# Performance work log

Measured on AMD Instinct MI355X. Metric: run time of the kernel, lower is better.

The kernel has to match this reference:

```python
import jax, jax.numpy as jnp
import numpy as np

EPS = 1e-6

def l2norm(x):
    return x / jnp.maximum(jnp.linalg.norm(x, axis=-1, keepdims=True), 1e-12)

def setup_inputs() -> dict:
    key = jax.random.key(0)
    ks = jax.random.split(key, 16)
    B, V, L = 64, 197, 64
    Dv, Dt, E = 768, 768, 256
    s = (2.0 / E) ** 0.5  # kaiming fan_out scale
    inp = {
        'visual_cls': jax.random.normal(ks[0], (B, Dv), jnp.float32),
        'textual_cls': jax.random.normal(ks[1], (B, Dt), jnp.float32),
        'visual_tokens': jax.random.normal(ks[2], (B, V, Dv), jnp.float32),
        'textual_tokens': jax.random.normal(ks[3], (B, L, Dt), jnp.float32),
        'text_length': jnp.maximum(jax.random.randint(ks[4], (B,), 0, L, jnp.int32), 1),
        'Wv': jax.random.normal(ks[5], (Dv, E), jnp.float32) * s,
        'bv': jnp.zeros((E,), jnp.float32),
        'Wt': jax.random.normal(ks[6], (Dt, E), jnp.float32) * s,
        'bt': jnp.zeros((E,), jnp.float32),
        'Wvt': jax.random.normal(ks[7], (Dv, E), jnp.float32) * s,
        'bvt': jnp.zeros((E,), jnp.float32),
        'Wtt': jax.random.normal(ks[8], (Dt, E), jnp.float32) * s,
        'btt': jnp.zeros((E,), jnp.float32),
    }
    return inp

def reference(visual_cls, textual_cls, visual_tokens, textual_tokens, text_length,
              Wv, bv, Wt, bt, Wvt, bvt, Wtt, btt):
    # cls projections
    v_cls = visual_cls @ Wv + bv            # [B, E]
    t_cls = textual_cls @ Wt + bt           # [B, E]
    # token projections + l2 normalize
    v_tok = l2norm(visual_tokens @ Wvt + bvt)   # [B, V, E]
    t_tok = l2norm(textual_tokens @ Wtt + btt)  # [B, L, E]
    B, V, E = v_tok.shape
    L = t_tok.shape[1]
    # full cross-modal token similarity (this is the kernel target)
    sim = jnp.einsum('bvd,qtd->bqvt', v_tok, t_tok)  # [B, Q, V, T]
    # image->text: max over text tokens, plain mean over visual tokens
    image_to_text = jnp.max(sim, axis=-1)            # [B, Q, V]
    image_to_text_sim = jnp.sum(image_to_text, axis=-1) / V  # [B, Q]
    # text->image: max over visual tokens, masked mean over text tokens
    text_to_image = jnp.max(sim, axis=-2)            # [B, Q, T]
    # faithful to original: mask indexed by FIRST batch axis b
    mask = jnp.arange(L)[None, :] >= text_length[:, None]   # [B, T]
    mask3 = mask[:, None, :]                                 # [B, 1, T]
    numer = jnp.sum(jnp.where(mask3, 0.0, text_to_image), axis=-1)
    denom = jnp.maximum(jnp.sum(~mask3, axis=-1).astype(text_to_image.dtype), EPS)
    text_to_image_sim = numer / denom                # [B, Q]
    return (v_cls, t_cls, image_to_text_sim, text_to_image_sim)
```

## Files before the change

### kernel.cpp

```cpp
#include <hip/hip_runtime.h>
#include <hip/hip_bf16.h>

#define NB 64
#define NV 197
#define NL 64
#define ND 768
#define NE 256

typedef __attribute__((ext_vector_type(8))) short bh8;
typedef __attribute__((ext_vector_type(16))) float f32x16;

__device__ inline ushort f2bf(float x) {
  __hip_bfloat16 h = __float2bfloat16(x);
  return *reinterpret_cast<ushort*>(&h);
}

__device__ inline bh8 cvt8(float4 a, float4 b) {
  union { bh8 v; ushort u[8]; } r;
  r.u[0] = f2bf(a.x); r.u[1] = f2bf(a.y); r.u[2] = f2bf(a.z); r.u[3] = f2bf(a.w);
  r.u[4] = f2bf(b.x); r.u[5] = f2bf(b.y); r.u[6] = f2bf(b.z); r.u[7] = f2bf(b.w);
  return r.v;
}

__global__ __launch_bounds__(128, 2) void proj_kernel(
    const float* __restrict__ Xv, const float* __restrict__ Xt,
    const float* __restrict__ Xcv, const float* __restrict__ Xct,
    const float* __restrict__ Wvt, const float* __restrict__ Wtt,
    const float* __restrict__ Wv, const float* __restrict__ Wt,
    const float* __restrict__ bvt, const float* __restrict__ btt,
    const float* __restrict__ bv, const float* __restrict__ bt,
    ushort* __restrict__ v_tok, ushort* __restrict__ t_tok,
    float* __restrict__ v_cls, float* __restrict__ t_cls) {
  __shared__ float ssq_lds[2][32];

  const int blk = blockIdx.x;
  const float* X; const float* W; const float* bias;
  ushort* outb = nullptr; float* outf = nullptr;
  int row0; bool norm;
  if (blk < 394)      { X = Xv;  W = Wvt; bias = bvt; outb = v_tok; row0 = blk * 32;         norm = true; }
  else if (blk < 522) { X = Xt;  W = Wtt; bias = btt; outb = t_tok; row0 = (blk - 394) * 32; norm = true; }
  else if (blk < 524) { X = Xcv; W = Wv;  bias = bv;  outf = v_cls; row0 = (blk - 522) * 32; norm = false; }
  else                { X = Xct; W = Wt;  bias = bt;  outf = t_cls; row0 = (blk - 524) * 32; norm = false; }

  const int tid = threadIdx.x;
  const int l = tid & 63, w = tid >> 6;
  const int lr = l & 31, hi = l >> 5;

  const float* Arow = X + (size_t)(row0 + lr) * ND + hi * 8;
  const float* Wcol = W + w * 128 + lr;

  f32x16 acc0 = {0}, acc1 = {0}, acc2 = {0}, acc3 = {0};

#pragma unroll 2
  for (int ks = 0; ks < 48; ++ks) {
    const float* Ak = Arow + ks * 16;
    float4 a0 = *(const float4*)Ak;
    float4 a1 = *(const float4*)(Ak + 4);
    bh8 af = cvt8(a0, a1);

    const float* Bk = Wcol + (size_t)(ks * 16 + hi * 8) * NE;
    union { bh8 v; ushort u[8]; } b0, b1, b2, b3;
#pragma unroll
    for (int e = 0; e < 8; ++e) {
      const float* Be = Bk + (size_t)e * NE;
      b0.u[e] = f2bf(Be[0]);
      b1.u[e] = f2bf(Be[32]);
      b2.u[e] = f2bf(Be[64]);
      b3.u[e] = f2bf(Be[96]);
    }
    acc0 = __builtin_amdgcn_mfma_f32_32x32x16_bf16(af, b0.v, acc0, 0, 0, 0);
    acc1 = __builtin_amdgcn_mfma_f32_32x32x16_bf16(af, b1.v, acc1, 0, 0, 0);
    acc2 = __builtin_amdgcn_mfma_f32_32x32x16_bf16(af, b2.v, acc2, 0, 0, 0);
    acc3 = __builtin_amdgcn_mfma_f32_32x32x16_bf16(af, b3.v, acc3, 0, 0, 0);
  }

  const float bn0 = bias[w * 128 + lr];
  const float bn1 = bias[w * 128 + 32 + lr];
  const float bn2 = bias[w * 128 + 64 + lr];
  const float bn3 = bias[w * 128 + 96 + lr];
#pragma unroll
  for (int r = 0; r < 16; ++r) {
    acc0[r] += bn0; acc1[r] += bn1; acc2[r] += bn2; acc3[r] += bn3;
  }

  if (norm) {
    float p[16];
#pragma unroll
    for (int r = 0; r < 16; ++r)
      p[r] = acc0[r] * acc0[r] + acc1[r] * acc1[r] +
             acc2[r] * acc2[r] + acc3[r] * acc3[r];
#pragma unroll
    for (int off = 1; off < 32; off <<= 1) {
#pragma unroll
      for (int r = 0; r < 16; ++r) p[r] += __shfl_xor(p[r], off);
    }
    if (lr == 0) {
#pragma unroll
      for (int r = 0; r < 16; ++r)
        ssq_lds[w][(r & 3) + 8 * (r >> 2) + 4 * hi] = p[r];
    }
    __syncthreads();
#pragma unroll
    for (int r = 0; r < 16; ++r) {
      const int R = (r & 3) + 8 * (r >> 2) + 4 * hi;
      const float s = ssq_lds[0][R] + ssq_lds[1][R];
      const float scale = 1.0f / fmaxf(sqrtf(s), 1e-12f);
      ushort* orow = outb + (size_t)(row0 + R) * NE + w * 128 + lr;
      orow[0]  = f2bf(acc0[r] * scale);
      orow[32] = f2bf(acc1[r] * scale);
      orow[64] = f2bf(acc2[r] * scale);
      orow[96] = f2bf(acc3[r] * scale);
    }
  } else {
#pragma unroll
    for (int r = 0; r < 16; ++r) {
      const int R = (r & 3) + 8 * (r >> 2) + 4 * hi;
      float* orow = outf + (size_t)(row0 + R) * NE + w * 128 + lr;
      orow[0]  = acc0[r];
      orow[32] = acc1[r];
      orow[64] = acc2[r];
      orow[96] = acc3[r];
    }
  }
}

__global__ __launch_bounds__(256, 2) void sim_kernel(
    const __hip_bfloat16* __restrict__ vt,
    const __hip_bfloat16* __restrict__ tt,
    const int* __restrict__ tlen,
    float* __restrict__ out_i2t,
    float* __restrict__ out_t2i) {
  __shared__ float red[4 * 64];
  __shared__ float wsum[4];

  const int blk = blockIdx.x;
  const int q = blk & 63;
  const int bc = blk >> 6;
  const int tid = threadIdx.x;
  const int l = tid & 63;
  const int w = tid >> 6;
  const int lr = l & 31;
  const int hi = l >> 5;

  bh8 breg0[16], breg1[16];
  {
    const __hip_bfloat16* T0 = tt + ((size_t)(q * NL) + lr) * NE + hi * 8;
    const __hip_bfloat16* T1 = T0 + 32 * NE;
#pragma unroll
    for (int s = 0; s < 16; ++s) {
      breg0[s] = *(const bh8*)(T0 + s * 16);
      breg1[s] = *(const bh8*)(T1 + s * 16);
    }
  }

  const int r0 = 32 * w + lr;
  const int r1 = min(128 + 32 * w + lr, NV - 1);

  for (int ib = 0; ib < 8; ++ib) {
    const int b = bc * 8 + ib;
    const __hip_bfloat16* Vb = vt + (size_t)b * NV * NE + hi * 8;
    const __hip_bfloat16* A0 = Vb + (size_t)r0 * NE;
    const __hip_bfloat16* A1 = Vb + (size_t)r1 * NE;

    f32x16 acc00 = {0}, acc01 = {0}, acc10 = {0}, acc11 = {0};

    bh8 a0[4], a1[4];
#pragma unroll
    for (int s = 0; s < 4; ++s) {
      a0[s] = *(const bh8*)(A0 + s * 16);
      a1[s] = *(const bh8*)(A1 + s * 16);
    }
#pragma unroll
    for (int s = 0; s < 16; ++s) {
      bh8 va0 = a0[s & 3], va1 = a1[s & 3];
      if (s < 12) {
        a0[s & 3] = *(const bh8*)(A0 + (s + 4) * 16);
        a1[s & 3] = *(const bh8*)(A1 + (s + 4) * 16);
      }
      acc00 = __builtin_amdgcn_mfma_f32_32x32x16_bf16(va0, breg0[s], acc00, 0, 0, 0);
      acc01 = __builtin_amdgcn_mfma_f32_32x32x16_bf16(va0, breg1[s], acc01, 0, 0, 0);
      acc10 = __builtin_amdgcn_mfma_f32_32x32x16_bf16(va1, breg0[s], acc10, 0, 0, 0);
      acc11 = __builtin_amdgcn_mfma_f32_32x32x16_bf16(va1, breg1[s], acc11, 0, 0, 0);
    }

    float i2t_sum = 0.0f;
#pragma unroll
    for (int r = 0; r < 16; ++r) {
      {
        float m = fmaxf(acc00[r], acc01[r]);
        m = fmaxf(m, __shfl_xor(m, 1));
        m = fmaxf(m, __shfl_xor(m, 2));
        m = fmaxf(m, __shfl_xor(m, 4));
        m = fmaxf(m, __shfl_xor(m, 8));
        m = fmaxf(m, __shfl_xor(m, 16));
        i2t_sum += m;
      }
      {
        float m = fmaxf(acc10[r], acc11[r]);
        m = fmaxf(m, __shfl_xor(m, 1));
        m = fmaxf(m, __shfl_xor(m, 2));
        m = fmaxf(m, __shfl_xor(m, 4));
        m = fmaxf(m, __shfl_xor(m, 8));
        m = fmaxf(m, __shfl_xor(m, 16));
        const int row = 128 + 32 * w + (r & 3) + 8 * (r >> 2) + 4 * hi;
        if (row < NV) i2t_sum += m;
      }
    }
    i2t_sum += __shfl_xor(i2t_sum, 32);
    if (l == 0) wsum[w] = i2t_sum;

    float vm0 = -1e30f, vm1 = -1e30f;
#pragma unroll
    for (int r = 0; r < 16; ++r) {
      vm0 = fmaxf(vm0, fmaxf(acc00[r], acc10[r]));
      vm1 = fmaxf(vm1, fmaxf(acc01[r], acc11[r]));
    }
    vm0 = fmaxf(vm0, __shfl_xor(vm0, 32));
    vm1 = fmaxf(vm1, __shfl_xor(vm1, 32));
    if (hi == 0) red[w * 64 + lr] = vm0;
    else         red[w * 64 + 32 + lr] = vm1;

    __syncthreads();

    if (tid < 64) {
      const int len = tlen[b];
      float m = fmaxf(fmaxf(red[tid], red[64 + tid]),
                      fmaxf(red[128 + tid], red[192 + tid]));
      float v = (tid < len) ? m : 0.0f;
#pragma unroll
      for (int off = 1; off < 64; off <<= 1) v += __shfl_xor(v, off);
      if (tid == 0) {
        out_t2i[b * NB + q] = v / fmaxf((float)len, 1e-6f);
        out_i2t[b * NB + q] = (wsum[0] + wsum[1] + wsum[2] + wsum[3]) / (float)NV;
      }
    }
    __syncthreads();
  }
}

extern "C" void kernel_launch(void* const* d_in, const int* in_sizes, int n_in,
                              void* d_out, int out_size, void* d_ws, size_t ws_size,
                              hipStream_t stream) {
  (void)in_sizes; (void)n_in; (void)out_size; (void)ws_size;
  const float* visual_cls    = (const float*)d_in[0];
  const float* textual_cls   = (const float*)d_in[1];
  const float* visual_tokens = (const float*)d_in[2];
  const float* textual_tokens= (const float*)d_in[3];
  const int*   text_length   = (const int*)d_in[4];
  const float* Wv  = (const float*)d_in[5];
  const float* bv  = (const float*)d_in[6];
  const float* Wt  = (const float*)d_in[7];
  const float* bt  = (const float*)d_in[8];
  const float* Wvt = (const float*)d_in[9];
  const float* bvt = (const float*)d_in[10];
  const float* Wtt = (const float*)d_in[11];
  const float* btt = (const float*)d_in[12];

  float* out   = (float*)d_out;
  float* v_cls = out;
  float* t_cls = out + NB * NE;
  float* i2t   = out + 2 * NB * NE;
  float* t2i   = i2t + NB * NB;

  ushort* wsb   = (ushort*)d_ws;
  ushort* v_tok = wsb;
  ushort* t_tok = v_tok + (size_t)NB * NV * NE;

  proj_kernel<<<526, 128, 0, stream>>>(visual_tokens, textual_tokens,
                                       visual_cls, textual_cls,
                                       Wvt, Wtt, Wv, Wt,
                                       bvt, btt, bv, bt,
                                       v_tok, t_tok, v_cls, t_cls);
  sim_kernel<<<NB * NB / 8, 256, 0, stream>>>((const __hip_bfloat16*)v_tok,
                                              (const __hip_bfloat16*)t_tok,
                                              text_length, i2t, t2i);
}
```

Before: 234.7 us.

## Pre-transpose weights to bf16 and pipeline sim kernel loads across batches

Adds a small kernel that converts the four fp32 weight matrices into transposed bf16 copies in workspace. The projection kernel can then fetch B operands as contiguous 16-byte vectors instead of 32 strided scalar loads with per-element conversion. The sim kernel now prefetches the next batch's visual rows while the current batch computes, raises wave priority around the MFMA loop, and defers the per-batch reductions to a single barrier at the end using larger shared buffers. The cost is one extra launch plus the weight conversion each call, and the last prefetch reads one batch past the block's range.

```diff
diff --git a/kernel.cpp b/kernel.cpp
--- a/kernel.cpp
+++ b/kernel.cpp
@@ -22,11 +22,45 @@
   return r.v;
 }
 
+__global__ __launch_bounds__(256) void wcvt_kernel(
+    const float* __restrict__ W0, const float* __restrict__ W1,
+    const float* __restrict__ W2, const float* __restrict__ W3,
+    ushort* __restrict__ O0, ushort* __restrict__ O1,
+    ushort* __restrict__ O2, ushort* __restrict__ O3) {
+  const float* Win; ushort* Wout;
+  switch (blockIdx.y) {
+    case 0: Win = W0; Wout = O0; break;
+    case 1: Win = W1; Wout = O1; break;
+    case 2: Win = W2; Wout = O2; break;
+    default: Win = W3; Wout = O3; break;
+  }
+  const int tk = blockIdx.x % 12, tn = blockIdx.x / 12;
+  const int k0 = tk * 64, n0 = tn * 64;
+  __shared__ ushort ts[64][72];
+  const int tid = threadIdx.x;
+#pragma unroll
+  for (int i = 0; i < 4; ++i) {
+    const int kl = (tid >> 4) + i * 16;
+    const int nl = (tid & 15) * 4;
+    float4 v = *(const float4*)&Win[(size_t)(k0 + kl) * NE + n0 + nl];
+    ts[nl + 0][kl] = f2bf(v.x);
+    ts[nl + 1][kl] = f2bf(v.y);
+    ts[nl + 2][kl] = f2bf(v.z);
+    ts[nl + 3][kl] = f2bf(v.w);
+  }
+  __syncthreads();
+  const int r = tid >> 2, c0 = (tid & 3) * 16;
+  bh8 v0 = *(const bh8*)&ts[r][c0];
+  bh8 v1 = *(const bh8*)&ts[r][c0 + 8];
+  *(bh8*)&Wout[(size_t)(n0 + r) * ND + k0 + c0] = v0;
+  *(bh8*)&Wout[(size_t)(n0 + r) * ND + k0 + c0 + 8] = v1;
+}
+
 __global__ __launch_bounds__(128, 2) void proj_kernel(
     const float* __restrict__ Xv, const float* __restrict__ Xt,
     const float* __restrict__ Xcv, const float* __restrict__ Xct,
-    const float* __restrict__ Wvt, const float* __restrict__ Wtt,
-    const float* __restrict__ Wv, const float* __restrict__ Wt,
+    const ushort* __restrict__ Wvt_t, const ushort* __restrict__ Wtt_t,
+    const ushort* __restrict__ Wv_t, const ushort* __restrict__ Wt_t,
     const float* __restrict__ bvt, const float* __restrict__ btt,
     const float* __restrict__ bv, const float* __restrict__ bt,
     ushort* __restrict__ v_tok, ushort* __restrict__ t_tok,
@@ -34,44 +68,39 @@
   __shared__ float ssq_lds[2][32];
 
   const int blk = blockIdx.x;
-  const float* X; const float* W; const float* bias;
+  const float* X; const ushort* W; const float* bias;
   ushort* outb = nullptr; float* outf = nullptr;
   int row0; bool norm;
-  if (blk < 394)      { X = Xv;  W = Wvt; bias = bvt; outb = v_tok; row0 = blk * 32;         norm = true; }
-  else if (blk < 522) { X = Xt;  W = Wtt; bias = btt; outb = t_tok; row0 = (blk - 394) * 32; norm = true; }
-  else if (blk < 524) { X = Xcv; W = Wv;  bias = bv;  outf = v_cls; row0 = (blk - 522) * 32; norm = false; }
-  else                { X = Xct; W = Wt;  bias = bt;  outf = t_cls; row0 = (blk - 524) * 32; norm = false; }
+  if (blk < 394)      { X = Xv;  W = Wvt_t; bias = bvt; outb = v_tok; row0 = blk * 32;         norm = true; }
+  else if (blk < 522) { X = Xt;  W = Wtt_t; bias = btt; outb = t_tok; row0 = (blk - 394) * 32; norm = true; }
+  else if (blk < 524) { X = Xcv; W = Wv_t;  bias = bv;  outf = v_cls; row0 = (blk - 522) * 32; norm = false; }
+  else                { X = Xct; W = Wt_t;  bias = bt;  outf = t_cls; row0 = (blk - 524) * 32; norm = false; }
 
   const int tid = threadIdx.x;
   const int l = tid & 63, w = tid >> 6;
   const int lr = l & 31, hi = l >> 5;
 
-  const float* Arow = X + (size_t)(row0 + lr) * ND + hi * 8;
-  const float* Wcol = W + w * 128 + lr;
+  const float*  Arow = X + (size_t)(row0 + lr) * ND + hi * 8;
+  const ushort* B0 = W + (size_t)(w * 128 + lr) * ND + hi * 8;
+  const ushort* B1 = B0 + 32 * ND;
+  const ushort* B2 = B0 + 64 * ND;
+  const ushort* B3 = B0 + 96 * ND;
 
   f32x16 acc0 = {0}, acc1 = {0}, acc2 = {0}, acc3 = {0};
 
-#pragma unroll 2
+#pragma unroll 4
   for (int ks = 0; ks < 48; ++ks) {
-    const float* Ak = Arow + ks * 16;
-    float4 a0 = *(const float4*)Ak;
-    float4 a1 = *(const float4*)(Ak + 4);
+    float4 a0 = *(const float4*)(Arow + ks * 16);
+    float4 a1 = *(const float4*)(Arow + ks * 16 + 4);
+    bh8 b0 = *(const bh8*)(B0 + ks * 16);
+    bh8 b1 = *(const bh8*)(B1 + ks * 16);
+    bh8 b2 = *(const bh8*)(B2 + ks * 16);
+    bh8 b3 = *(const bh8*)(B3 + ks * 16);
     bh8 af = cvt8(a0, a1);
-
-    const float* Bk = Wcol + (size_t)(ks * 16 + hi * 8) * NE;
-    union { bh8 v; ushort u[8]; } b0, b1, b2, b3;
-#pragma unroll
-    for (int e = 0; e < 8; ++e) {
-      const float* Be = Bk + (size_t)e * NE;
-      b0.u[e] = f2bf(Be[0]);
-      b1.u[e] = f2bf(Be[32]);
-      b2.u[e] = f2bf(Be[64]);
-      b3.u[e] = f2bf(Be[96]);
-    }
-    acc0 = __builtin_amdgcn_mfma_f32_32x32x16_bf16(af, b0.v, acc0, 0, 0, 0);
-    acc1 = __builtin_amdgcn_mfma_f32_32x32x16_bf16(af, b1.v, acc1, 0, 0, 0);
-    acc2 = __builtin_amdgcn_mfma_f32_32x32x16_bf16(af, b2.v, acc2, 0, 0, 0);
-    acc3 = __builtin_amdgcn_mfma_f32_32x32x16_bf16(af, b3.v, acc3, 0, 0, 0);
+    acc0 = __builtin_amdgcn_mfma_f32_32x32x16_bf16(af, b0, acc0, 0, 0, 0);
+    acc1 = __builtin_amdgcn_mfma_f32_32x32x16_bf16(af, b1, acc1, 0, 0, 0);
+    acc2 = __builtin_amdgcn_mfma_f32_32x32x16_bf16(af, b2, acc2, 0, 0, 0);
+    acc3 = __builtin_amdgcn_mfma_f32_32x32x16_bf16(af, b3, acc3, 0, 0, 0);
   }
 
   const float bn0 = bias[w * 128 + lr];
@@ -130,8 +159,8 @@
     const int* __restrict__ tlen,
     float* __restrict__ out_i2t,
     float* __restrict__ out_t2i) {
-  __shared__ float red[4 * 64];
-  __shared__ float wsum[4];
+  __shared__ float red[8][4][64];
+  __shared__ float wsum[8][4];
 
   const int blk = blockIdx.x;
   const int q = blk & 63;
@@ -141,6 +170,7 @@
   const int w = tid >> 6;
   const int lr = l & 31;
   const int hi = l >> 5;
+  const size_t bstride = (size_t)NV * NE;
 
   bh8 breg0[16], breg1[16];
   {
@@ -156,32 +186,35 @@
   const int r0 = 32 * w + lr;
   const int r1 = min(128 + 32 * w + lr, NV - 1);
 
+  const __hip_bfloat16* A0 = vt + (size_t)(bc * 8) * bstride + (size_t)r0 * NE + hi * 8;
+  const __hip_bfloat16* A1 = vt + (size_t)(bc * 8) * bstride + (size_t)r1 * NE + hi * 8;
+
+  bh8 a0[4], a1[4];
+#pragma unroll
+  for (int s = 0; s < 4; ++s) {
+    a0[s] = *(const bh8*)(A0 + s * 16);
+    a1[s] = *(const bh8*)(A1 + s * 16);
+  }
+
   for (int ib = 0; ib < 8; ++ib) {
-    const int b = bc * 8 + ib;
-    const __hip_bfloat16* Vb = vt + (size_t)b * NV * NE + hi * 8;
-    const __hip_bfloat16* A0 = Vb + (size_t)r0 * NE;
-    const __hip_bfloat16* A1 = Vb + (size_t)r1 * NE;
-
     f32x16 acc00 = {0}, acc01 = {0}, acc10 = {0}, acc11 = {0};
 
-    bh8 a0[4], a1[4];
-#pragma unroll
-    for (int s = 0; s < 4; ++s) {
-      a0[s] = *(const bh8*)(A0 + s * 16);
-      a1[s] = *(const bh8*)(A1 + s * 16);
-    }
+    __builtin_amdgcn_s_setprio(1);
 #pragma unroll
     for (int s = 0; s < 16; ++s) {
       bh8 va0 = a0[s & 3], va1 = a1[s & 3];
-      if (s < 12) {
-        a0[s & 3] = *(const bh8*)(A0 + (s + 4) * 16);
-        a1[s & 3] = *(const bh8*)(A1 + (s + 4) * 16);
-      }
+      const int sn = s + 4;
+      const size_t off = (size_t)(sn & 15) * 16 + (size_t)(sn >> 4) * bstride;
+      a0[s & 3] = *(const bh8*)(A0 + off);
+      a1[s & 3] = *(const bh8*)(A1 + off);
       acc00 = __builtin_amdgcn_mfma_f32_32x32x16_bf16(va0, breg0[s], acc00, 0, 0, 0);
       acc01 = __builtin_amdgcn_mfma_f32_32x32x16_bf16(va0, breg1[s], acc01, 0, 0, 0);
       acc10 = __builtin_amdgcn_mfma_f32_32x32x16_bf16(va1, breg0[s], acc10, 0, 0, 0);
       acc11 = __builtin_amdgcn_mfma_f32_32x32x16_bf16(va1, breg1[s], acc11, 0, 0, 0);
     }
+    __builtin_amdgcn_s_setprio(0);
+    A0 += bstride;
+    A1 += bstride;
 
     float i2t_sum = 0.0f;
 #pragma unroll
@@ -207,7 +240,7 @@
       }
     }
     i2t_sum += __shfl_xor(i2t_sum, 32);
-    if (l == 0) wsum[w] = i2t_sum;
+    if (l == 0) wsum[ib][w] = i2t_sum;
 
     float vm0 = -1e30f, vm1 = -1e30f;
 #pragma unroll
@@ -217,24 +250,27 @@
     }
     vm0 = fmaxf(vm0, __shfl_xor(vm0, 32));
     vm1 = fmaxf(vm1, __shfl_xor(vm1, 32));
-    if (hi == 0) red[w * 64 + lr] = vm0;
-    else         red[w * 64 + 32 + lr] = vm1;
-
-    __syncthreads();
-
-    if (tid < 64) {
-      const int len = tlen[b];
-      float m = fmaxf(fmaxf(red[tid], red[64 + tid]),
-                      fmaxf(red[128 + tid], red[192 + tid]));
-      float v = (tid < len) ? m : 0.0f;
-#pragma unroll
-      for (int off = 1; off < 64; off <<= 1) v += __shfl_xor(v, off);
-      if (tid == 0) {
-        out_t2i[b * NB + q] = v / fmaxf((float)len, 1e-6f);
-        out_i2t[b * NB + q] = (wsum[0] + wsum[1] + wsum[2] + wsum[3]) / (float)NV;
-      }
-    }
-    __syncthreads();
+    if (hi == 0) red[ib][w][lr] = vm0;
+    else         red[ib][w][32 + lr] = vm1;
+  }
+
+  __syncthreads();
+
+#pragma unroll
+  for (int j = 0; j < 2; ++j) {
+    const int ib = w * 2 + j;
+    const int b = bc * 8 + ib;
+    const int len = tlen[b];
+    float m = fmaxf(fmaxf(red[ib][0][l], red[ib][1][l]),
+                    fmaxf(red[ib][2][l], red[ib][3][l]));
+    float v = (l < len) ? m : 0.0f;
+#pragma unroll
+    for (int off = 1; off < 64; off <<= 1) v += __shfl_xor(v, off);
+    if (l == 0) {
+      out_t2i[b * NB + q] = v / fmaxf((float)len, 1e-6f);
+      out_i2t[b * NB + q] = (wsum[ib][0] + wsum[ib][1] +
+                             wsum[ib][2] + wsum[ib][3]) / (float)NV;
+    }
   }
 }
 
@@ -265,10 +301,16 @@
   ushort* wsb   = (ushort*)d_ws;
   ushort* v_tok = wsb;
   ushort* t_tok = v_tok + (size_t)NB * NV * NE;
-
+  ushort* Wvt_t = t_tok + (size_t)NB * NL * NE;
+  ushort* Wtt_t = Wvt_t + (size_t)NE * ND;
+  ushort* Wv_t  = Wtt_t + (size_t)NE * ND;
+  ushort* Wt_t  = Wv_t  + (size_t)NE * ND;
+
+  wcvt_kernel<<<dim3(48, 4), 256, 0, stream>>>(Wvt, Wtt, Wv, Wt,
+                                               Wvt_t, Wtt_t, Wv_t, Wt_t);
   proj_kernel<<<526, 128, 0, stream>>>(visual_tokens, textual_tokens,
                                        visual_cls, textual_cls,
-                                       Wvt, Wtt, Wv, Wt,
+                                       Wvt_t, Wtt_t, Wv_t, Wt_t,
                                        bvt, btt, bv, bt,
                                        v_tok, t_tok, v_cls, t_cls);
   sim_kernel<<<NB * NB / 8, 256, 0, stream>>>((const __hip_bfloat16*)v_tok,
```

Measured after the change: 237.7 us. About the same (+1.3%).
